# Optimization experiments

Measured on AMD Instinct MI355X. Metric: run time of the kernel, lower is better.

The kernel has to match this reference:

```python
import jax, jax.numpy as jnp
import numpy as np

LABEL_NC = 35
S_DIM = 64
DIM_IN = 64
NHIDDEN = 128
CLASS_SELECTED = np.array([24, 25, 26, 27, 28, 29, 30, 31, 32, 33])


def conv3x3(x, w, b):
    # x: [B,C,H,W], w: [O,I,3,3] -> [B,O,H,W], padding=1
    y = jax.lax.conv_general_dilated(x, w, window_strides=(1, 1), padding='SAME',
                                     dimension_numbers=('NCHW', 'OIHW', 'NCHW'))
    return y + b[None, :, None, None]


def lrelu(x, slope=0.2):
    return jnp.where(x >= 0, x, slope * x)


def setup_inputs() -> dict:
    key = jax.random.key(0)
    ks = jax.random.split(key, 16)
    B, H, W = 8, 256, 256
    featmap_in = jax.random.normal(ks[0], (B, DIM_IN, H, W), jnp.float32)
    seg_labels = jax.random.randint(ks[1], (B, H, W), 0, LABEL_NC)
    bg_mask = (jax.random.uniform(ks[2], (B, 1, H, W)) < 0.9).astype(jnp.float32)
    mask = (jax.random.uniform(ks[3], (B, 1, H, W)) < 0.3).astype(jnp.float32)

    def w(k, o, i):
        return jax.random.normal(k, (o, i, 3, 3), jnp.float32) * (1.0 / np.sqrt(i * 9))

    spade_in = S_DIM + LABEL_NC  # 99
    return {
        'featmap_in': featmap_in, 'seg_labels': seg_labels, 'bg_mask': bg_mask, 'mask': mask,
        'w_conv': w(ks[4], S_DIM, DIM_IN), 'b_conv': jnp.zeros((S_DIM,), jnp.float32),
        'w_c0': w(ks[5], DIM_IN, DIM_IN), 'b_c0': jnp.zeros((DIM_IN,), jnp.float32),
        'w_sh': w(ks[6], NHIDDEN, spade_in), 'b_sh': jnp.zeros((NHIDDEN,), jnp.float32),
        'w_g': w(ks[7], DIM_IN, NHIDDEN), 'b_g': jnp.zeros((DIM_IN,), jnp.float32),
        'w_b': w(ks[8], DIM_IN, NHIDDEN), 'b_b': jnp.zeros((DIM_IN,), jnp.float32),
    }


def reference(featmap_in, seg_labels, bg_mask, mask,
              w_conv, b_conv, w_c0, b_c0, w_sh, b_sh, w_g, b_g, w_b, b_b):
    dtype = featmap_in.dtype
    segmap = jax.nn.one_hot(seg_labels, LABEL_NC, axis=1, dtype=dtype)  # [B,S,H,W]

    # Conv2dBlock(norm='none', activation='lrelu')
    featmap = lrelu(conv3x3(featmap_in, w_conv, b_conv))  # [B,F,H,W], F=S_DIM

    # interpolation to featmap spatial size is identity here (same H,W)
    ctx_segmap = segmap * bg_mask * (1.0 - mask)
    bg_segmap = segmap * bg_mask

    # fused per-(batch,class) masked mean pooling (replaces python double loop)
    m = (ctx_segmap > 0).astype(dtype)                       # [B,S,H,W]
    sums = jnp.einsum('bshw,bfhw->bsf', m, featmap)          # [B,S,F]
    cnts = m.sum(axis=(2, 3))[..., None]                     # [B,S,1]
    codes = jnp.where(cnts > 0, sums / jnp.maximum(cnts, 1.0), 0.0)
    keep = jnp.ones((LABEL_NC,), dtype).at[jnp.asarray(CLASS_SELECTED)].set(0.0)
    codes_vector = codes * keep[None, :, None]               # [B,S,F]

    # style_map = codes^T @ bg_segmap, broadcast codes back onto the map
    style_map = jnp.einsum('bsf,bshw->bfhw', codes_vector, bg_segmap)  # [B,F,H,W]
    out_map = jnp.concatenate([style_map, bg_segmap], axis=1)          # [B,F+S,H,W]

    # StyleLayer: conv -> SPADE -> lrelu
    dx = conv3x3(featmap_in, w_c0, b_c0)
    mu = dx.mean(axis=(2, 3), keepdims=True)
    var = ((dx - mu) ** 2).mean(axis=(2, 3), keepdims=True)
    normalized = (dx - mu) * jax.lax.rsqrt(var + 1e-5)       # param-free instance norm
    actv = jax.nn.relu(conv3x3(out_map, w_sh, b_sh))
    gamma = conv3x3(actv, w_g, b_g)
    beta = conv3x3(actv, w_b, b_b)
    out = lrelu(normalized * (1.0 + gamma) + beta)
    return out
```

## Files before the change

### kernel.cpp

```cpp
#include <hip/hip_runtime.h>
#include <hip/hip_bf16.h>
#include <cstdint>

#define Bn 8
#define Hh 256
#define Ww 256
#define HW 65536
#define SDIM 64
#define LABELS 35
#define NHID 128
#define CLB ((size_t)Hh * 16 * 256 * 16)

typedef __attribute__((ext_vector_type(8))) short bf16x8;
typedef __attribute__((ext_vector_type(4))) float f32x4;
#define MFMA16 __builtin_amdgcn_mfma_f32_16x16x32_bf16

__device__ __forceinline__ void gll16(const void* g, void* l) {
    __builtin_amdgcn_global_load_lds(
        (__attribute__((address_space(1))) const void*)(uintptr_t)g,
        (__attribute__((address_space(3))) void*)(uint32_t)(uintptr_t)l, 16, 0, 0);
}

#define TUNITS (3 * 4 * 260)

__device__ __forceinline__ void stageCL(bf16x8* tile, const char* clb, int jo0,
                                        int h, int t, const float* zrow) {
    const int wv = t >> 6, l = t & 63;
#pragma unroll
    for (int i = 0; i < 12; i++) {
        int k = wv * 12 + i;
        int r = k >> 4, rem = k & 15, s = rem >> 2, q = rem & 3;
        int gh = h + r - 1;
        const char* src = ((unsigned)gh < Hh)
            ? clb + ((((size_t)gh * 16 + jo0 + s) * 256) + (size_t)q * 64 + l) * 16
            : (const char*)zrow + l * 16;
        gll16(src, tile + (r * 4 + s) * 260 + 1 + q * 64);
    }
}

__device__ __forceinline__ bf16x8 bread(const bf16x8* tile, int ky, int kx,
                                        int pt, int wv, int l) {
    return tile[(ky * 4 + (l >> 4)) * 260 + wv * 64 + pt * 16 + (l & 15) + kx];
}

__device__ __forceinline__ bf16x8 aread(const ushort* base, int blk, int loff) {
    return *(const bf16x8*)((const char*)base + ((size_t)blk << 10) + loff);
}
__device__ __forceinline__ int blkC(int ocbI, int mat, int half, int tap) {
    return (((ocbI * 4 + mat) * 2 + half) * 9 + tap);
}

__global__ __launch_bounds__(256) void repack_fin(
    const float* __restrict__ fin, char* __restrict__ fincl, int batch0)
{
    __shared__ __align__(16) float fs[64 * 256];
    const int t = threadIdx.x, h = blockIdx.x, z = blockIdx.y;
    const int b = batch0 + z;
    const int wv = t >> 6, l = t & 63;
    const float* finb = fin + (size_t)b * 64 * HW + (size_t)h * 256;
#pragma unroll
    for (int i = 0; i < 16; i++) {
        int ic = wv * 16 + i;
        gll16(finb + (size_t)ic * HW + l * 4, fs + ic * 256);
    }
    __syncthreads();
    char* outb = fincl + (size_t)z * CLB + (size_t)h * 16 * 256 * 16;
#pragma unroll
    for (int jo = 0; jo < 8; jo++) {
        uint hi[4], lo[4];
#pragma unroll
        for (int c = 0; c < 8; c += 2) {
            float v0 = fs[(jo * 8 + c) * 256 + t];
            float v1 = fs[(jo * 8 + c + 1) * 256 + t];
            __hip_bfloat16 h0 = __float2bfloat16(v0), h1 = __float2bfloat16(v1);
            float r0 = v0 - __bfloat162float(h0), r1 = v1 - __bfloat162float(h1);
            __hip_bfloat16 l0 = __float2bfloat16(r0), l1 = __float2bfloat16(r1);
            hi[c >> 1] = (uint)*(ushort*)&h0 | ((uint)*(ushort*)&h1 << 16);
            lo[c >> 1] = (uint)*(ushort*)&l0 | ((uint)*(ushort*)&l1 << 16);
        }
        *(uint4*)(outb + ((size_t)jo * 256 + t) * 16)       = make_uint4(hi[0], hi[1], hi[2], hi[3]);
        *(uint4*)(outb + ((size_t)(jo + 8) * 256 + t) * 16) = make_uint4(lo[0], lo[1], lo[2], lo[3]);
    }
}

__global__ void prep_wfragC(const float* __restrict__ w1, const float* __restrict__ w0,
                            ushort* __restrict__ dst) {
    const int N = 288 * 512;
    for (int idx = blockIdx.x * blockDim.x + threadIdx.x; idx < N; idx += gridDim.x * blockDim.x) {
        int k = idx & 31, oc = (idx >> 5) & 15;
        int blk = idx >> 9;
        int tap = blk % 9, r = blk / 9;
        int half = r & 1; r >>= 1;
        int mat = r & 3; int ocbI = r >> 2;
        int OC = ocbI * 16 + oc, ic = half * 32 + k;
        const float* w = (mat < 2) ? w1 : w0;
        float v = w[((size_t)OC * 64 + ic) * 9 + tap];
        __hip_bfloat16 h16 = __float2bfloat16(v);
        if (mat & 1) { float rr = v - __bfloat162float(h16); h16 = __float2bfloat16(rr); }
        dst[idx] = *(ushort*)&h16;
    }
}

__global__ void prep_wfrag(const float* __restrict__ wg, const float* __restrict__ wb2,
                           ushort* __restrict__ dst) {
    const int N = 16 * 36 * 512;
    for (int idx = blockIdx.x * blockDim.x + threadIdx.x; idx < N; idx += gridDim.x * blockDim.x) {
        int k = idx & 31, oc = (idx >> 5) & 15;
        int blk = idx >> 9;
        int ks = blk % 36, q = blk / 36;
        int ocbI = q & 3, q4 = q >> 2, hl = q4 & 1, mat = q4 >> 1;
        int icq = ks / 9, tap = ks % 9;
        int OC = ocbI * 16 + oc, ic = icq * 32 + k;
        const float* w = mat ? wb2 : wg;
        float v = w[((size_t)OC * 128 + ic) * 9 + tap];
        __hip_bfloat16 h16 = __float2bfloat16(v);
        if (hl) { float r = v - __bfloat162float(h16); h16 = __float2bfloat16(r); }
        dst[idx] = *(ushort*)&h16;
    }
}

__global__ __launch_bounds__(256) void conv1c0_kernel(
    const char* __restrict__ fincl, const ushort* __restrict__ wfC,
    const float* __restrict__ bias1, const float* __restrict__ bias0,
    const int* __restrict__ seg, const float* __restrict__ bg,
    const float* __restrict__ mask, const float* __restrict__ zrow,
    float* __restrict__ sums, int* __restrict__ cnts, float* __restrict__ statacc,
    int batch0)
{
    __shared__ __align__(16) bf16x8 tile[TUNITS];
    __shared__ float s35[LABELS * 16];
    __shared__ int   c35[LABELS];
    __shared__ float wsum[4][16][2];

    const int t = threadIdx.x, h = blockIdx.y, bxI = blockIdx.x, ocb = bxI * 16;
    const int z = blockIdx.z, b = batch0 + z;
    const int l = t & 63, wv = t >> 6;
    const char* clb = fincl + (size_t)z * CLB;
    const int loff = ((l & 15) << 6) + ((l >> 4) << 4);

    for (int i = t; i < LABELS * 16; i += 256) s35[i] = 0.f;
    if (t < LABELS) c35[t] = 0;
    if (t < 24) { int r = t >> 3, s = (t >> 1) & 3, e = t & 1;
        bf16x8 zz = {0,0,0,0,0,0,0,0};
        tile[(r * 4 + s) * 260 + (e ? 257 : 0)] = zz; }

    f32x4 a1[4], a0[4];
#pragma unroll
    for (int j = 0; j < 4; j++) {
        int c = ocb + ((l >> 4) << 2) + j;
        float v1 = bias1[c], v0 = bias0[c];
#pragma unroll
        for (int pt = 0; pt < 4; pt++) { a1[pt][j] = v1; a0[pt][j] = v0; }
    }

#pragma unroll
    for (int icq = 0; icq < 4; icq++) {
        stageCL(tile, clb, icq * 4, h, t, zrow);
        __syncthreads();
#pragma unroll
        for (int tap = 0; tap < 9; tap++) {
            const int ky = tap / 3, kx = tap % 3;
            if (icq < 2) {
                bf16x8 A0 = aread(wfC, blkC(bxI, 0, icq, tap), loff);
                bf16x8 A1 = aread(wfC, blkC(bxI, 1, icq, tap), loff);
                bf16x8 A2 = aread(wfC, blkC(bxI, 2, icq, tap), loff);
                bf16x8 A3 = aread(wfC, blkC(bxI, 3, icq, tap), loff);
#pragma unroll
                for (int pt = 0; pt < 4; pt++) {
                    bf16x8 B = bread(tile, ky, kx, pt, wv, l);
                    a1[pt] = MFMA16(A0, B, a1[pt], 0, 0, 0);
                    a1[pt] = MFMA16(A1, B, a1[pt], 0, 0, 0);
                    a0[pt] = MFMA16(A2, B, a0[pt], 0, 0, 0);
                    a0[pt] = MFMA16(A3, B, a0[pt], 0, 0, 0);
                }
            } else {
                bf16x8 A0 = aread(wfC, blkC(bxI, 0, icq - 2, tap), loff);
                bf16x8 A2 = aread(wfC, blkC(bxI, 2, icq - 2, tap), loff);
#pragma unroll
                for (int pt = 0; pt < 4; pt++) {
                    bf16x8 B = bread(tile, ky, kx, pt, wv, l);
                    a1[pt] = MFMA16(A0, B, a1[pt], 0, 0, 0);
                    a0[pt] = MFMA16(A2, B, a0[pt], 0, 0, 0);
                }
            }
        }
        __syncthreads();
    }

    const int*   segh = seg  + (size_t)b * HW + (size_t)h * 256;
    const float* bgh  = bg   + (size_t)b * HW + (size_t)h * 256;
    const float* mh   = mask + (size_t)b * HW + (size_t)h * 256;
#pragma unroll
    for (int pt = 0; pt < 4; pt++) {
        int px = wv * 64 + pt * 16 + (l & 15);
        int lab = segh[px];
        bool m = (bgh[px] != 0.f) && (mh[px] == 0.f);
        if (m) {
#pragma unroll
            for (int j = 0; j < 4; j++) {
                float o = a1[pt][j];
                o = (o >= 0.f) ? o : 0.2f * o;
                atomicAdd(&s35[lab * 16 + ((l >> 4) << 2) + j], o);
            }
            if (bxI == 0 && l < 16) atomicAdd(&c35[lab], 1);
        }
    }
#pragma unroll
    for (int j = 0; j < 4; j++) {
        float s = a0[0][j] + a0[1][j] + a0[2][j] + a0[3][j];
        float ss = a0[0][j]*a0[0][j] + a0[1][j]*a0[1][j] + a0[2][j]*a0[2][j] + a0[3][j]*a0[3][j];
#pragma unroll
        for (int off = 1; off < 16; off <<= 1) { s += __shfl_xor(s, off); ss += __shfl_xor(ss, off); }
        if ((l & 15) == 0) { wsum[wv][((l >> 4) << 2) + j][0] = s; wsum[wv][((l >> 4) << 2) + j][1] = ss; }
    }
    __syncthreads();
    for (int i = t; i < LABELS * 16; i += 256) {
        float v = s35[i];
        if (v != 0.f) {
            int s = i >> 4, oc = i & 15;
            atomicAdd(&sums[((size_t)b * LABELS + s) * SDIM + ocb + oc], v);
        }
    }
    if (bxI == 0 && t < LABELS && c35[t] > 0) atomicAdd(&cnts[b * LABELS + t], c35[t]);
    if (t < 16) {
        float S = 0.f, SS = 0.f;
#pragma unroll
        for (int w2 = 0; w2 < 4; w2++) { S += wsum[w2][t][0]; SS += wsum[w2][t][1]; }
        atomicAdd(&statacc[(size_t)(b * SDIM + ocb + t) * 2 + 0], S);
        atomicAdd(&statacc[(size_t)(b * SDIM + ocb + t) * 2 + 1], SS);
    }
}

__global__ void codes_kernel(const float* __restrict__ sums, const int* __restrict__ cnts,
                             float* __restrict__ codes) {
    int idx = blockIdx.x * blockDim.x + threadIdx.x;
    if (idx >= Bn * LABELS * SDIM) return;
    int s  = (idx >> 6) % LABELS;
    int bs = idx >> 6;
    int cnt = cnts[bs];
    bool keep = !(s >= 24 && s <= 33);
    codes[idx] = (cnt > 0 && keep) ? sums[idx] / (float)cnt : 0.f;
}

__global__ void finalize_stats(const float* __restrict__ statacc,
                               float* __restrict__ mu, float* __restrict__ rsig) {
    int i = blockIdx.x * blockDim.x + threadIdx.x;
    if (i >= Bn * SDIM) return;
    float S = statacc[2 * i], SS = statacc[2 * i + 1];
    float m = S / (float)HW;
    float v = SS / (float)HW - m * m;
    mu[i] = m;
    rsig[i] = rsqrtf(v + 1e-5f);
}

__global__ void make_T(const float* __restrict__ codes, const float* __restrict__ w_sh,
                       float* __restrict__ T) {
    __shared__ float cod[64];
    const int lab = blockIdx.x, b = blockIdx.y, t = threadIdx.x;
    if (t < 64) cod[t] = codes[((size_t)b * LABELS + lab) * SDIM + t];
    __syncthreads();
    for (int i = t; i < NHID * 9; i += 256) {
        int oc = i / 9, tap = i % 9;
        float s = w_sh[((size_t)oc * 99 + 64 + lab) * 9 + tap];
#pragma unroll
        for (int ic = 0; ic < 64; ic++)
            s = fmaf(w_sh[((size_t)oc * 99 + ic) * 9 + tap], cod[ic], s);
        T[((size_t)b * NHID + oc) * (LABELS * 9) + lab * 9 + tap] = s;
    }
}

__global__ __launch_bounds__(256) void conv_sh_kernel(
    const int* __restrict__ seg, const float* __restrict__ bg,
    const float* __restrict__ T, const float* __restrict__ bf,
    char* __restrict__ actv, int batch0)
{
    __shared__ float Ts[16 * 316];
    __shared__ int   labr[3 * 260];
    __shared__ float bgr[3 * 260];

    const int t = threadIdx.x, h = blockIdx.y, bxI = blockIdx.x, ocb = bxI * 16;
    const int z = blockIdx.z, b = batch0 + z;
    const int*   seg_b = seg + (size_t)b * HW;
    const float* bg_b  = bg + (size_t)b * HW;
    char* actv_b = actv + (size_t)z * CLB;

    const float* Tb = T + ((size_t)b * NHID + ocb) * 315;
    for (int i = t; i < 16 * 315; i += 256)
        Ts[(i / 315) * 316 + (i % 315)] = Tb[i];

    for (int i = t; i < 3 * 258; i += 256) {
        int r = i / 258, x = i % 258;
        int gh = h + r - 1, gw = x - 1;
        int lab = 0; float bgv = 0.f;
        if ((unsigned)gh < Hh && (unsigned)gw < Ww) { lab = seg_b[gh * Ww + gw]; bgv = bg_b[gh * Ww + gw]; }
        labr[r * 260 + x] = lab; bgr[r * 260 + x] = bgv;
    }

    float acc[16];
#pragma unroll
    for (int oc = 0; oc < 16; oc++) acc[oc] = bf[ocb + oc];
    __syncthreads();

#pragma unroll
    for (int ky = 0; ky < 3; ky++) {
#pragma unroll
        for (int kx = 0; kx < 3; kx++) {
            int lab  = labr[ky * 260 + t + kx];
            float bgv = bgr[ky * 260 + t + kx];
            int off = lab * 9 + ky * 3 + kx;
#pragma unroll
            for (int oc = 0; oc < 16; oc++)
                acc[oc] = fmaf(Ts[oc * 316 + off], bgv, acc[oc]);
        }
    }

    uint pk[8];
#pragma unroll
    for (int i = 0; i < 8; i++) {
        float lo = fmaxf(acc[2 * i], 0.f), hi = fmaxf(acc[2 * i + 1], 0.f);
        __hip_bfloat16 l16 = __float2bfloat16(lo), h16 = __float2bfloat16(hi);
        pk[i] = (uint)*(ushort*)&l16 | ((uint)*(ushort*)&h16 << 16);
    }
    *(uint4*)(actv_b + (((size_t)h * 16 + bxI * 2)     * 256 + t) * 16) = make_uint4(pk[0], pk[1], pk[2], pk[3]);
    *(uint4*)(actv_b + (((size_t)h * 16 + bxI * 2 + 1) * 256 + t) * 16) = make_uint4(pk[4], pk[5], pk[6], pk[7]);
}

__global__ __launch_bounds__(256) void final_fused_kernel(
    const char* __restrict__ fincl, const char* __restrict__ actv,
    const ushort* __restrict__ wfC, const ushort* __restrict__ wfGB,
    const float* __restrict__ bc0, const float* __restrict__ bg2, const float* __restrict__ bb2,
    const float* __restrict__ mu, const float* __restrict__ rsig,
    const float* __restrict__ zrow, float* __restrict__ out, int batch0)
{
    __shared__ __align__(16) bf16x8 tile[TUNITS];
    const int t = threadIdx.x, h = blockIdx.y, bxI = blockIdx.x, ocb = bxI * 16;
    const int z = blockIdx.z, b = batch0 + z;
    const int l = t & 63, wv = t >> 6;
    const char* clb = fincl + (size_t)z * CLB;
    const char* avb = actv + (size_t)z * CLB;
    const int loff = ((l & 15) << 6) + ((l >> 4) << 4);

    if (t < 24) { int r = t >> 3, s = (t >> 1) & 3, e = t & 1;
        bf16x8 zz = {0,0,0,0,0,0,0,0};
        tile[(r * 4 + s) * 260 + (e ? 257 : 0)] = zz; }

    f32x4 ad[4], ag[4], ab2[4];
#pragma unroll
    for (int j = 0; j < 4; j++) {
        int c = ocb + ((l >> 4) << 2) + j;
        float vd = bc0[c], vg = bg2[c], vb = bb2[c];
#pragma unroll
        for (int pt = 0; pt < 4; pt++) { ad[pt][j] = vd; ag[pt][j] = vg; ab2[pt][j] = vb; }
    }

#pragma unroll
    for (int c8 = 0; c8 < 8; c8++) {
        const bool isfin = (c8 < 4);
        const int icq = isfin ? c8 : c8 - 4;
        stageCL(tile, isfin ? clb : avb, icq * 4, h, t, zrow);
        __syncthreads();
#pragma unroll
        for (int tap = 0; tap < 9; tap++) {
            const int ky = tap / 3, kx = tap % 3;
            if (isfin) {
                if (icq < 2) {
                    bf16x8 A2 = aread(wfC, blkC(bxI, 2, icq, tap), loff);
                    bf16x8 A3 = aread(wfC, blkC(bxI, 3, icq, tap), loff);
#pragma unroll
                    for (int pt = 0; pt < 4; pt++) {
                        bf16x8 B = bread(tile, ky, kx, pt, wv, l);
                        ad[pt] = MFMA16(A2, B, ad[pt], 0, 0, 0);
                        ad[pt] = MFMA16(A3, B, ad[pt], 0, 0, 0);
                    }
                } else {
                    bf16x8 A2 = aread(wfC, blkC(bxI, 2, icq - 2, tap), loff);
#pragma unroll
                    for (int pt = 0; pt < 4; pt++) {
                        bf16x8 B = bread(tile, ky, kx, pt, wv, l);
                        ad[pt] = MFMA16(A2, B, ad[pt], 0, 0, 0);
                    }
                }
            } else {
                const int ks = icq * 9 + tap;
                bf16x8 agh = aread(wfGB, (0 * 4 + bxI) * 36 + ks, loff);
                bf16x8 agl = aread(wfGB, (1 * 4 + bxI) * 36 + ks, loff);
                bf16x8 abh = aread(wfGB, (2 * 4 + bxI) * 36 + ks, loff);
                bf16x8 abl = aread(wfGB, (3 * 4 + bxI) * 36 + ks, loff);
#pragma unroll
                for (int pt = 0; pt < 4; pt++) {
                    bf16x8 B = bread(tile, ky, kx, pt, wv, l);
                    ag[pt]  = MFMA16(agh, B, ag[pt], 0, 0, 0);
                    ag[pt]  = MFMA16(agl, B, ag[pt], 0, 0, 0);
                    ab2[pt] = MFMA16(abh, B, ab2[pt], 0, 0, 0);
                    ab2[pt] = MFMA16(abl, B, ab2[pt], 0, 0, 0);
                }
            }
        }
        __syncthreads();
    }

    const float* mu_b = mu + b * SDIM;
    const float* rs_b = rsig + b * SDIM;
    float* out_b = out + (size_t)b * SDIM * HW;
    float muj[4], rsj[4];
#pragma unroll
    for (int j = 0; j < 4; j++) { int c = ocb + ((l >> 4) << 2) + j; muj[j] = mu_b[c]; rsj[j] = rs_b[c]; }
#pragma unroll
    for (int pt = 0; pt < 4; pt++) {
        int px = wv * 64 + pt * 16 + (l & 15);
#pragma unroll
        for (int j = 0; j < 4; j++) {
            int cl = ((l >> 4) << 2) + j;
            float nrm = (ad[pt][j] - muj[j]) * rsj[j];
            float o = nrm * (1.f + ag[pt][j]) + ab2[pt][j];
            o = (o >= 0.f) ? o : 0.2f * o;
            out_b[(size_t)(ocb + cl) * HW + (size_t)h * 256 + px] = o;
        }
    }
}

extern "C" void kernel_launch(void* const* d_in, const int* in_sizes, int n_in,
                              void* d_out, int out_size, void* d_ws, size_t ws_size,
                              hipStream_t stream) {
    const float* featmap_in = (const float*)d_in[0];
    const int*   seg        = (const int*)d_in[1];
    const float* bg         = (const float*)d_in[2];
    const float* mask       = (const float*)d_in[3];
    const float* w_conv     = (const float*)d_in[4];
    const float* b_conv     = (const float*)d_in[5];
    const float* w_c0       = (const float*)d_in[6];
    const float* b_c0       = (const float*)d_in[7];
    const float* w_sh       = (const float*)d_in[8];
    const float* b_sh       = (const float*)d_in[9];
    const float* w_g        = (const float*)d_in[10];
    const float* b_g        = (const float*)d_in[11];
    const float* w_b        = (const float*)d_in[12];
    const float* b_b        = (const float*)d_in[13];
    float* out = (float*)d_out;

    char* ws = (char*)d_ws;
    size_t o = 0;
    auto alloc = [&](size_t bytes) -> char* {
        size_t r = o; o = (o + bytes + 255) & ~(size_t)255; return ws + r;
    };
    ushort* wfC     = (ushort*)alloc((size_t)288 * 512 * 2);
    ushort* wfGB    = (ushort*)alloc((size_t)16 * 36 * 512 * 2);
    float*  Ttab    = (float*)alloc((size_t)Bn * NHID * LABELS * 9 * 4);
    float*  sums    = (float*)alloc((size_t)Bn * LABELS * SDIM * 4);
    int*    cnts    = (int*)alloc((size_t)Bn * LABELS * 4);
    float*  codes   = (float*)alloc((size_t)Bn * LABELS * SDIM * 4);
    float*  statacc = (float*)alloc((size_t)Bn * SDIM * 2 * 4);
    float*  mu      = (float*)alloc((size_t)Bn * SDIM * 4);
    float*  rsig    = (float*)alloc((size_t)Bn * SDIM * 4);
    float*  zrow    = (float*)alloc(1024);

    size_t rem = (ws_size > o) ? ws_size - o : 0;
    int tier = (rem >= 2 * CLB * Bn + 1024) ? 1 : (rem >= CLB * Bn + CLB + 1024) ? 2 : 3;
    char* fincl; char* actvc;
    if (tier == 1)      { fincl = alloc(CLB * Bn); actvc = alloc(CLB * Bn); }
    else if (tier == 2) { fincl = alloc(CLB * Bn); actvc = alloc(CLB); }
    else                { fincl = alloc(CLB);      actvc = alloc(CLB); }

    prep_wfragC<<<144, 256, 0, stream>>>(w_conv, w_c0, wfC);
    prep_wfrag<<<288, 256, 0, stream>>>(w_g, w_b, wfGB);

    hipMemsetAsync(sums, 0, (size_t)Bn * LABELS * SDIM * 4, stream);
    hipMemsetAsync(cnts, 0, (size_t)Bn * LABELS * 4, stream);
    hipMemsetAsync(statacc, 0, (size_t)Bn * SDIM * 2 * 4, stream);
    hipMemsetAsync(zrow, 0, 1024, stream);

    if (tier <= 2) {
        repack_fin<<<dim3(Hh, Bn), 256, 0, stream>>>(featmap_in, fincl, 0);
        conv1c0_kernel<<<dim3(4, Hh, Bn), 256, 0, stream>>>(
            fincl, wfC, b_conv, b_c0, seg, bg, mask, zrow, sums, cnts, statacc, 0);
    } else {
        for (int b = 0; b < Bn; b++) {
            repack_fin<<<dim3(Hh, 1), 256, 0, stream>>>(featmap_in, fincl, b);
            conv1c0_kernel<<<dim3(4, Hh, 1), 256, 0, stream>>>(
                fincl, wfC, b_conv, b_c0, seg, bg, mask, zrow, sums, cnts, statacc, b);
        }
    }
    codes_kernel<<<(Bn * LABELS * SDIM + 255) / 256, 256, 0, stream>>>(sums, cnts, codes);
    finalize_stats<<<2, 256, 0, stream>>>(statacc, mu, rsig);
    make_T<<<dim3(LABELS, Bn), 256, 0, stream>>>(codes, w_sh, Ttab);

    if (tier == 1) {
        conv_sh_kernel<<<dim3(8, Hh, Bn), 256, 0, stream>>>(seg, bg, Ttab, b_sh, actvc, 0);
        final_fused_kernel<<<dim3(4, Hh, Bn), 256, 0, stream>>>(
            fincl, actvc, wfC, wfGB, b_c0, b_g, b_b, mu, rsig, zrow, out, 0);
    } else if (tier == 2) {
        for (int b = 0; b < Bn; b++) {
            conv_sh_kernel<<<dim3(8, Hh, 1), 256, 0, stream>>>(seg, bg, Ttab, b_sh, actvc, b);
            final_fused_kernel<<<dim3(4, Hh, 1), 256, 0, stream>>>(
                fincl + (size_t)b * CLB, actvc, wfC, wfGB, b_c0, b_g, b_b, mu, rsig, zrow, out, b);
        }
    } else {
        for (int b = 0; b < Bn; b++) {
            repack_fin<<<dim3(Hh, 1), 256, 0, stream>>>(featmap_in, fincl, b);
            conv_sh_kernel<<<dim3(8, Hh, 1), 256, 0, stream>>>(seg, bg, Ttab, b_sh, actvc, b);
            final_fused_kernel<<<dim3(4, Hh, 1), 256, 0, stream>>>(
                fincl, actvc, wfC, wfGB, b_c0, b_g, b_b, mu, rsig, zrow, out, b);
        }
    }
}
```

Before: 1.511 ms.

## Replace LDS tile staging with direct global B-operand loads in conv kernels

Removes the shared-memory halo tile, along with its global_load_lds staging and the block barriers, from the conv1c0 and final fused kernels. Each lane now reads its bf16x8 B operand straight from global memory (which the L1/L2 caches serve), and out-of-bounds pixels read from a zero row. This cuts LDS use and synchronisation, which may raise occupancy. In exchange, every tap (9 per channel group) issues its own global load, so the same data is fetched repeatedly and the kernels become more exposed to memory latency.

```diff
diff --git a/kernel.cpp b/kernel.cpp
--- a/kernel.cpp
+++ b/kernel.cpp
@@ -21,26 +21,11 @@
         (__attribute__((address_space(3))) void*)(uint32_t)(uintptr_t)l, 16, 0, 0);
 }
 
-#define TUNITS (3 * 4 * 260)
-
-__device__ __forceinline__ void stageCL(bf16x8* tile, const char* clb, int jo0,
-                                        int h, int t, const float* zrow) {
-    const int wv = t >> 6, l = t & 63;
-#pragma unroll
-    for (int i = 0; i < 12; i++) {
-        int k = wv * 12 + i;
-        int r = k >> 4, rem = k & 15, s = rem >> 2, q = rem & 3;
-        int gh = h + r - 1;
-        const char* src = ((unsigned)gh < Hh)
-            ? clb + ((((size_t)gh * 16 + jo0 + s) * 256) + (size_t)q * 64 + l) * 16
-            : (const char*)zrow + l * 16;
-        gll16(src, tile + (r * 4 + s) * 260 + 1 + q * 64);
-    }
-}
-
-__device__ __forceinline__ bf16x8 bread(const bf16x8* tile, int ky, int kx,
-                                        int pt, int wv, int l) {
-    return tile[(ky * 4 + (l >> 4)) * 260 + wv * 64 + pt * 16 + (l & 15) + kx];
+__device__ __forceinline__ bf16x8 breadG(const char* rowp, bool rok, int px,
+                                         const char* zp) {
+    bool ok = rok && ((unsigned)px < Ww);
+    const char* src = ok ? rowp + (size_t)px * 16 : zp;
+    return *(const bf16x8*)src;
 }
 
 __device__ __forceinline__ bf16x8 aread(const ushort* base, int blk, int loff) {
@@ -127,7 +112,6 @@
     float* __restrict__ sums, int* __restrict__ cnts, float* __restrict__ statacc,
     int batch0)
 {
-    __shared__ __align__(16) bf16x8 tile[TUNITS];
     __shared__ float s35[LABELS * 16];
     __shared__ int   c35[LABELS];
     __shared__ float wsum[4][16][2];
@@ -136,13 +120,13 @@
     const int z = blockIdx.z, b = batch0 + z;
     const int l = t & 63, wv = t >> 6;
     const char* clb = fincl + (size_t)z * CLB;
+    const char* zp = (const char*)zrow;
     const int loff = ((l & 15) << 6) + ((l >> 4) << 4);
+    const int myoct = l >> 4;
+    const int pxb = wv * 64 + (l & 15);
 
     for (int i = t; i < LABELS * 16; i += 256) s35[i] = 0.f;
     if (t < LABELS) c35[t] = 0;
-    if (t < 24) { int r = t >> 3, s = (t >> 1) & 3, e = t & 1;
-        bf16x8 zz = {0,0,0,0,0,0,0,0};
-        tile[(r * 4 + s) * 260 + (e ? 257 : 0)] = zz; }
 
     f32x4 a1[4], a0[4];
 #pragma unroll
@@ -155,11 +139,13 @@
 
 #pragma unroll
     for (int icq = 0; icq < 4; icq++) {
-        stageCL(tile, clb, icq * 4, h, t, zrow);
-        __syncthreads();
+        const int jo0 = icq * 4;
 #pragma unroll
         for (int tap = 0; tap < 9; tap++) {
             const int ky = tap / 3, kx = tap % 3;
+            const int gh = h + ky - 1;
+            const bool rok = (unsigned)gh < Hh;
+            const char* rowp = clb + ((size_t)gh * 16 + jo0 + myoct) * (256 * 16);
             if (icq < 2) {
                 bf16x8 A0 = aread(wfC, blkC(bxI, 0, icq, tap), loff);
                 bf16x8 A1 = aread(wfC, blkC(bxI, 1, icq, tap), loff);
@@ -167,7 +153,7 @@
                 bf16x8 A3 = aread(wfC, blkC(bxI, 3, icq, tap), loff);
 #pragma unroll
                 for (int pt = 0; pt < 4; pt++) {
-                    bf16x8 B = bread(tile, ky, kx, pt, wv, l);
+                    bf16x8 B = breadG(rowp, rok, pxb + pt * 16 + kx - 1, zp);
                     a1[pt] = MFMA16(A0, B, a1[pt], 0, 0, 0);
                     a1[pt] = MFMA16(A1, B, a1[pt], 0, 0, 0);
                     a0[pt] = MFMA16(A2, B, a0[pt], 0, 0, 0);
@@ -178,13 +164,12 @@
                 bf16x8 A2 = aread(wfC, blkC(bxI, 2, icq - 2, tap), loff);
 #pragma unroll
                 for (int pt = 0; pt < 4; pt++) {
-                    bf16x8 B = bread(tile, ky, kx, pt, wv, l);
+                    bf16x8 B = breadG(rowp, rok, pxb + pt * 16 + kx - 1, zp);
                     a1[pt] = MFMA16(A0, B, a1[pt], 0, 0, 0);
                     a0[pt] = MFMA16(A2, B, a0[pt], 0, 0, 0);
                 }
             }
         }
-        __syncthreads();
     }
 
     const int*   segh = seg  + (size_t)b * HW + (size_t)h * 256;
@@ -332,17 +317,15 @@
     const float* __restrict__ mu, const float* __restrict__ rsig,
     const float* __restrict__ zrow, float* __restrict__ out, int batch0)
 {
-    __shared__ __align__(16) bf16x8 tile[TUNITS];
     const int t = threadIdx.x, h = blockIdx.y, bxI = blockIdx.x, ocb = bxI * 16;
     const int z = blockIdx.z, b = batch0 + z;
     const int l = t & 63, wv = t >> 6;
     const char* clb = fincl + (size_t)z * CLB;
     const char* avb = actv + (size_t)z * CLB;
+    const char* zp = (const char*)zrow;
     const int loff = ((l & 15) << 6) + ((l >> 4) << 4);
-
-    if (t < 24) { int r = t >> 3, s = (t >> 1) & 3, e = t & 1;
-        bf16x8 zz = {0,0,0,0,0,0,0,0};
-        tile[(r * 4 + s) * 260 + (e ? 257 : 0)] = zz; }
+    const int myoct = l >> 4;
+    const int pxb = wv * 64 + (l & 15);
 
     f32x4 ad[4], ag[4], ab2[4];
 #pragma unroll
@@ -357,18 +340,21 @@
     for (int c8 = 0; c8 < 8; c8++) {
         const bool isfin = (c8 < 4);
         const int icq = isfin ? c8 : c8 - 4;
-        stageCL(tile, isfin ? clb : avb, icq * 4, h, t, zrow);
-        __syncthreads();
+        const char* tb = isfin ? clb : avb;
+        const int jo0 = icq * 4;
 #pragma unroll
         for (int tap = 0; tap < 9; tap++) {
             const int ky = tap / 3, kx = tap % 3;
+            const int gh = h + ky - 1;
+            const bool rok = (unsigned)gh < Hh;
+            const char* rowp = tb + ((size_t)gh * 16 + jo0 + myoct) * (256 * 16);
             if (isfin) {
                 if (icq < 2) {
                     bf16x8 A2 = aread(wfC, blkC(bxI, 2, icq, tap), loff);
                     bf16x8 A3 = aread(wfC, blkC(bxI, 3, icq, tap), loff);
 #pragma unroll
                     for (int pt = 0; pt < 4; pt++) {
-                        bf16x8 B = bread(tile, ky, kx, pt, wv, l);
+                        bf16x8 B = breadG(rowp, rok, pxb + pt * 16 + kx - 1, zp);
                         ad[pt] = MFMA16(A2, B, ad[pt], 0, 0, 0);
                         ad[pt] = MFMA16(A3, B, ad[pt], 0, 0, 0);
                     }
@@ -376,7 +362,7 @@
                     bf16x8 A2 = aread(wfC, blkC(bxI, 2, icq - 2, tap), loff);
 #pragma unroll
                     for (int pt = 0; pt < 4; pt++) {
-                        bf16x8 B = bread(tile, ky, kx, pt, wv, l);
+                        bf16x8 B = breadG(rowp, rok, pxb + pt * 16 + kx - 1, zp);
                         ad[pt] = MFMA16(A2, B, ad[pt], 0, 0, 0);
                     }
                 }
@@ -388,7 +374,7 @@
                 bf16x8 abl = aread(wfGB, (3 * 4 + bxI) * 36 + ks, loff);
 #pragma unroll
                 for (int pt = 0; pt < 4; pt++) {
-                    bf16x8 B = bread(tile, ky, kx, pt, wv, l);
+                    bf16x8 B = breadG(rowp, rok, pxb + pt * 16 + kx - 1, zp);
                     ag[pt]  = MFMA16(agh, B, ag[pt], 0, 0, 0);
                     ag[pt]  = MFMA16(agl, B, ag[pt], 0, 0, 0);
                     ab2[pt] = MFMA16(abh, B, ab2[pt], 0, 0, 0);
@@ -396,7 +382,6 @@
                 }
             }
         }
-        __syncthreads();
     }
 
     const float* mu_b = mu + b * SDIM;
```

Result: slower. 2.275 ms (+50.5%).
